# Optimization experiments

Measured on AMD Instinct MI355X. Metric: run time of the kernel, lower is better.

## Reference

```python
import jax, jax.numpy as jnp
import numpy as np

L, D, H, DH, DF = 4, 512, 8, 64, 2048
B, S = 4, 2048
EPS = 1e-6  # fast-transformers causal-linear eps


def _ln(x, g, b, eps=1e-5):
    mu = jnp.mean(x, axis=-1, keepdims=True)
    var = jnp.var(x, axis=-1, keepdims=True)
    return (x - mu) * jax.lax.rsqrt(var + eps) * g + b


def _causal_linear(Q, K, V):
    # Q, K, V: [B, S, H, DH]; O(N) linear-attention recurrence over S
    Qs = jnp.moveaxis(Q, 1, 0)
    Ks = jnp.moveaxis(K, 1, 0)
    Vs = jnp.moveaxis(V, 1, 0)
    b = Q.shape[0]
    kv0 = jnp.zeros((b, H, DH, DH), Q.dtype)  # running sum of k v^T
    z0 = jnp.zeros((b, H, DH), Q.dtype)       # running sum of k

    def step(carry, qkv):
        kv, z = carry
        q, k, v = qkv  # each [B, H, DH]
        kv = kv + k[..., :, None] * v[..., None, :]
        z = z + k
        num = jnp.einsum('bhd,bhdm->bhm', q, kv)
        den = jnp.einsum('bhd,bhd->bh', q, z) + EPS
        return (kv, z), num / den[..., None]

    _, out = jax.lax.scan(step, (kv0, z0), (Qs, Ks, Vs))
    return jnp.moveaxis(out, 0, 1)  # [B, S, H, DH]


def _layer(x, p):
    Wq, bq, Wk, bk, Wv, bv, Wo, bo, W1, b1, W2, b2, g1, be1, g2, be2 = p
    b, s, _ = x.shape
    q = (x @ Wq + bq).reshape(b, s, H, DH)
    k = (x @ Wk + bk).reshape(b, s, H, DH)
    v = (x @ Wv + bv).reshape(b, s, H, DH)
    Qf = jax.nn.elu(q) + 1.0  # feature map phi(x) = elu(x) + 1
    Kf = jax.nn.elu(k) + 1.0
    a = _causal_linear(Qf, Kf, v).reshape(b, s, D)
    x = x + (a @ Wo + bo)            # residual (dropout=0)
    x = _ln(x, g1, be1)              # post-norm
    y = jax.nn.gelu(x @ W1 + b1, approximate=False) @ W2 + b2
    return _ln(x + y, g2, be2)


def _encoder(h, params, gf, bef):
    def body(x, p):
        return _layer(x, p), None
    x, _ = jax.lax.scan(body, h, params)
    return _ln(x, gf, bef)  # final LayerNorm from builder


def setup_inputs() -> dict:
    key = jax.random.key(0)
    ks = jax.random.split(key, 8)

    def w(k, shape, fan_in):
        return jax.random.normal(k, shape, jnp.float32) * (fan_in ** -0.5)

    return {
        'h': jax.random.normal(ks[0], (B, S, D), jnp.float32),
        'Wq': w(ks[1], (L, D, D), D), 'bq': jnp.zeros((L, D), jnp.float32),
        'Wk': w(ks[2], (L, D, D), D), 'bk': jnp.zeros((L, D), jnp.float32),
        'Wv': w(ks[3], (L, D, D), D), 'bv': jnp.zeros((L, D), jnp.float32),
        'Wo': w(ks[4], (L, D, D), D), 'bo': jnp.zeros((L, D), jnp.float32),
        'W1': w(ks[5], (L, D, DF), D), 'b1': jnp.zeros((L, DF), jnp.float32),
        'W2': w(ks[6], (L, DF, D), DF), 'b2': jnp.zeros((L, D), jnp.float32),
        'g1': jnp.ones((L, D), jnp.float32), 'be1': jnp.zeros((L, D), jnp.float32),
        'g2': jnp.ones((L, D), jnp.float32), 'be2': jnp.zeros((L, D), jnp.float32),
        'gf': jnp.ones((D,), jnp.float32), 'bef': jnp.zeros((D,), jnp.float32),
    }


def reference(h, Wq, bq, Wk, bk, Wv, bv, Wo, bo, W1, b1, W2, b2,
              g1, be1, g2, be2, gf, bef):
    params = (Wq, bq, Wk, bk, Wv, bv, Wo, bo, W1, b1, W2, b2, g1, be1, g2, be2)
    return _encoder(h, params, gf, bef)
```

## Files before the change

kernel.cpp:

```cpp
#include <hip/hip_runtime.h>
#include <hip/hip_bf16.h>
#include <math.h>

#define LAYERS 4
#define DMODEL 512
#define NH 8
#define DH 64
#define DFF 2048
#define NB 4
#define S_LEN 2048
#define MROWS 8192
#define CHUNK 64
#define NCHUNK 32
#define ATT_EPS 1e-6f
#define LN_EPS 1e-5f
#define SEGSTRIDE (MROWS * DMODEL)

typedef __attribute__((ext_vector_type(8))) short short8v;
typedef __attribute__((ext_vector_type(4))) float f32x4;

__device__ __forceinline__ float b2f(unsigned short u) {
    union { float f; unsigned u; } c; c.u = ((unsigned)u) << 16; return c.f;
}
__device__ __forceinline__ unsigned short f2b(float f) {
    union { float f; unsigned u; } c; c.f = f;
    unsigned r = c.u + 0x7FFFu + ((c.u >> 16) & 1u);
    return (unsigned short)(r >> 16);
}
__device__ __forceinline__ void gload16(const void* g, void* l) {
    __builtin_amdgcn_global_load_lds(
        (const __attribute__((address_space(1))) void*)g,
        (__attribute__((address_space(3))) void*)l, 16, 0, 0);
}
__device__ __forceinline__ float elu1f(float v) {
    return (v > 0.f) ? (v + 1.f) : __expf(v);
}
__device__ __forceinline__ float geluf(float v) {
    float u = 0.7978845608028654f * v * (1.f + 0.044715f * v * v);
    float th = 1.f - 2.f / (1.f + __expf(2.f * u));
    return 0.5f * v * (1.f + th);
}

template <int ACT, bool ACCUM, bool ATOMIC, bool WF32, bool WBF16, int KSPLIT>
__global__ __launch_bounds__(512, 4) void gemm8(
    const unsigned short* __restrict__ A,
    const unsigned short* __restrict__ WT,
    const float* __restrict__ b0, const float* __restrict__ b1,
    const float* __restrict__ b2,
    float* __restrict__ C32, unsigned short* __restrict__ Cbf,
    int M, int N, int K)
{
    __shared__ short S[2][16384];

    const int t = threadIdx.x;
    const int m0 = blockIdx.x * 128, n0 = blockIdx.y * 128;
    const int kz = (KSPLIT > 1) ? blockIdx.z : 0;
    const int Kc = K / KSPLIT;
    const int kbeg = kz * Kc;
    const int lane = t & 63, wid = t >> 6;
    const int wm = (wid >> 2) * 64;
    const int wn = (wid & 3) * 32;
    const int fr = lane & 15, kg = lane >> 4;

    const unsigned short* gsrc[4];
    int ldso[4];
#pragma unroll
    for (int r = 0; r < 4; ++r) {
        const int u = (r & 1) ? (t + 512) : t;
        const bool isA = (r < 2);
        const int row = u >> 3, sp = u & 7, sl = sp ^ (row & 7);
        gsrc[r] = (isA ? A + (size_t)(m0 + row) * K
                       : WT + (size_t)(n0 + row) * K) + kbeg + sl * 8;
        ldso[r] = (isA ? 0 : 8192) + u * 8;
    }

    int aoff[2][4], boff[2][2];
#pragma unroll
    for (int h = 0; h < 2; ++h) {
#pragma unroll
        for (int m = 0; m < 4; ++m) {
            const int R = wm + m * 16 + fr;
            aoff[h][m] = R * 64 + (((h * 4 + kg) ^ (R & 7)) * 8);
        }
#pragma unroll
        for (int n = 0; n < 2; ++n) {
            const int R = wn + n * 16 + fr;
            boff[h][n] = 8192 + R * 64 + (((h * 4 + kg) ^ (R & 7)) * 8);
        }
    }

    f32x4 acc[4][2];
#pragma unroll
    for (int m = 0; m < 4; ++m)
#pragma unroll
        for (int n = 0; n < 2; ++n) acc[m][n] = (f32x4){0.f, 0.f, 0.f, 0.f};

#define STAGE(b, kt) do { _Pragma("unroll")                                  \
    for (int r = 0; r < 4; ++r)                                              \
        gload16(gsrc[r] + (size_t)(kt) * 64, &S[b][ldso[r]]); } while (0)

    const int NT = Kc >> 6;
    STAGE(0, 0);

    for (int td = 0; td < NT; ++td) {
        const int b = td & 1;
        if (td + 1 < NT) {
            STAGE(b ^ 1, td + 1);
            __builtin_amdgcn_sched_barrier(0);
            asm volatile("s_waitcnt vmcnt(4)");
        } else {
            __builtin_amdgcn_sched_barrier(0);
            asm volatile("s_waitcnt vmcnt(0)");
        }
        __builtin_amdgcn_sched_barrier(0);
        __builtin_amdgcn_s_barrier();
        __builtin_amdgcn_sched_barrier(0);

        short8v a0[4], b0f[2], a1[4], b1f[2];
#pragma unroll
        for (int m = 0; m < 4; ++m) a0[m] = *(const short8v*)&S[b][aoff[0][m]];
#pragma unroll
        for (int n = 0; n < 2; ++n) b0f[n] = *(const short8v*)&S[b][boff[0][n]];
#pragma unroll
        for (int m = 0; m < 4; ++m) a1[m] = *(const short8v*)&S[b][aoff[1][m]];
#pragma unroll
        for (int n = 0; n < 2; ++n) b1f[n] = *(const short8v*)&S[b][boff[1][n]];

        asm volatile("s_waitcnt lgkmcnt(6)");
        __builtin_amdgcn_sched_barrier(0);
        __builtin_amdgcn_s_setprio(1);
#pragma unroll
        for (int m = 0; m < 4; ++m)
#pragma unroll
            for (int n = 0; n < 2; ++n)
                acc[m][n] = __builtin_amdgcn_mfma_f32_16x16x32_bf16(
                    a0[m], b0f[n], acc[m][n], 0, 0, 0);
        __builtin_amdgcn_s_setprio(0);

        asm volatile("s_waitcnt lgkmcnt(0)");
        __builtin_amdgcn_sched_barrier(0);
        __builtin_amdgcn_s_setprio(1);
#pragma unroll
        for (int m = 0; m < 4; ++m)
#pragma unroll
            for (int n = 0; n < 2; ++n)
                acc[m][n] = __builtin_amdgcn_mfma_f32_16x16x32_bf16(
                    a1[m], b1f[n], acc[m][n], 0, 0, 0);
        __builtin_amdgcn_s_setprio(0);

        __builtin_amdgcn_sched_barrier(0);
        __builtin_amdgcn_s_barrier();
    }
#undef STAGE

    const int seg = (ACT == 3) ? (n0 >> 9) : 0;
    const float* bias = (ACT == 3) ? (seg == 0 ? b0 : (seg == 1 ? b1 : b2)) : b0;
    float bv[2];
#pragma unroll
    for (int n = 0; n < 2; ++n) {
        const int col = n0 + wn + n * 16 + fr;
        bv[n] = bias[(ACT == 3) ? (col - seg * 512) : col];
    }
    if (KSPLIT > 1 && kz != 0) { bv[0] = 0.f; bv[1] = 0.f; }

#pragma unroll
    for (int m = 0; m < 4; ++m)
#pragma unroll
        for (int n = 0; n < 2; ++n)
#pragma unroll
            for (int j = 0; j < 4; ++j) {
                const int row = m0 + wm + m * 16 + (lane >> 4) * 4 + j;
                const int col = n0 + wn + n * 16 + fr;
                float v = acc[m][n][j] + bv[n];
                if (ACCUM) v += C32[(size_t)row * N + col];
                if (ACT == 1) v = elu1f(v);
                else if (ACT == 2) v = geluf(v);
                else if (ACT == 3) { if (seg < 2) v = elu1f(v); }
                if (ATOMIC) {
                    atomicAdd(&C32[(size_t)row * N + col], v);
                } else {
                    if (WF32) C32[(size_t)row * N + col] = v;
                }
                if (WBF16) {
                    if (ACT == 3)
                        Cbf[(size_t)seg * SEGSTRIDE + (size_t)row * 512 + (col - seg * 512)] = f2b(v);
                    else
                        Cbf[(size_t)row * N + col] = f2b(v);
                }
            }
}

__global__ __launch_bounds__(256) void transpose_to_bf16(
    const float* __restrict__ W, unsigned short* __restrict__ WT, int K, int N)
{
    __shared__ float tile[32][33];
    const int k0 = blockIdx.x * 32, n0 = blockIdx.y * 32;
    const int tx = threadIdx.x & 31, ty = threadIdx.x >> 5;
#pragma unroll
    for (int i = ty; i < 32; i += 8)
        tile[i][tx] = W[(size_t)(k0 + i) * N + n0 + tx];
    __syncthreads();
#pragma unroll
    for (int i = ty; i < 32; i += 8)
        WT[(size_t)(n0 + i) * K + k0 + tx] = f2b(tile[tx][i]);
}

__global__ __launch_bounds__(256) void cvt_in(
    const float* __restrict__ h, float* __restrict__ x,
    unsigned short* __restrict__ xb, int n)
{
    const int i = (blockIdx.x * 256 + threadIdx.x) * 8;
    if (i >= n) return;
    f32x4 a = *(const f32x4*)(h + i);
    f32x4 b = *(const f32x4*)(h + i + 4);
    *(f32x4*)(x + i) = a;
    *(f32x4*)(x + i + 4) = b;
    short8v p;
    p[0] = f2b(a[0]); p[1] = f2b(a[1]); p[2] = f2b(a[2]); p[3] = f2b(a[3]);
    p[4] = f2b(b[0]); p[5] = f2b(b[1]); p[6] = f2b(b[2]); p[7] = f2b(b[3]);
    *(short8v*)(xb + i) = p;
}

__device__ __forceinline__ int swzo(int row, int sl) {
    return row * 64 + ((sl ^ (row & 7)) << 3);
}

__global__ __launch_bounds__(256) void attn_stage1(
    const unsigned short* __restrict__ Kf, const unsigned short* __restrict__ Vf,
    unsigned short* __restrict__ KVp, float* __restrict__ zp)
{
    const int c = blockIdx.x, hh = blockIdx.y, bb = blockIdx.z;
    const int t = threadIdx.x;
    const int lane = t & 63, w = t >> 6;
    const int fr = lane & 15, g = lane >> 4;

    __shared__ unsigned short KTs[64 * 72];
    __shared__ unsigned short VTs[64 * 72];

    const size_t rowbase = (size_t)(bb * S_LEN + c * CHUNK);
    const int colbase = hh * DH;

    {
        const int r = lane, cs = w * 16;
        const unsigned short* kp = Kf + (rowbase + r) * DMODEL + colbase + cs;
        const unsigned short* vp = Vf + (rowbase + r) * DMODEL + colbase + cs;
        short8v k0 = *(const short8v*)kp, k1 = *(const short8v*)(kp + 8);
        short8v v0 = *(const short8v*)vp, v1 = *(const short8v*)(vp + 8);
#pragma unroll
        for (int i = 0; i < 8; ++i) {
            KTs[(cs + i) * 72 + r]     = (unsigned short)k0[i];
            KTs[(cs + 8 + i) * 72 + r] = (unsigned short)k1[i];
            VTs[(cs + i) * 72 + r]     = (unsigned short)v0[i];
            VTs[(cs + 8 + i) * 72 + r] = (unsigned short)v1[i];
        }
    }
    __syncthreads();

    f32x4 cacc[4];
#pragma unroll
    for (int nf = 0; nf < 4; ++nf) cacc[nf] = (f32x4){0.f, 0.f, 0.f, 0.f};

    const short8v a0 = *(const short8v*)&VTs[(w * 16 + fr) * 72 + g * 8];
    const short8v a1 = *(const short8v*)&VTs[(w * 16 + fr) * 72 + (4 + g) * 8];
#pragma unroll
    for (int nf = 0; nf < 4; ++nf) {
        short8v bq0 = *(const short8v*)&KTs[(nf * 16 + fr) * 72 + g * 8];
        short8v bq1 = *(const short8v*)&KTs[(nf * 16 + fr) * 72 + (4 + g) * 8];
        cacc[nf] = __builtin_amdgcn_mfma_f32_16x16x32_bf16(a0, bq0, cacc[nf], 0, 0, 0);
        cacc[nf] = __builtin_amdgcn_mfma_f32_16x16x32_bf16(a1, bq1, cacc[nf], 0, 0, 0);
    }

    const size_t base = ((size_t)(bb * NH + hh) * NCHUNK + c) * (DH * DH);
#pragma unroll
    for (int nf = 0; nf < 4; ++nf)
#pragma unroll
        for (int reg = 0; reg < 4; ++reg) {
            const int e = w * 16 + g * 4 + reg;
            const int d = nf * 16 + fr;
            KVp[base + e * 64 + d] = f2b(cacc[nf][reg]);
        }

    if (t < 64) {
        float s = 0.f;
#pragma unroll
        for (int sl = 0; sl < 8; ++sl) {
            short8v kv = *(const short8v*)&KTs[t * 72 + sl * 8];
#pragma unroll
            for (int i = 0; i < 8; ++i) s += b2f((unsigned short)kv[i]);
        }
        zp[((size_t)(bb * NH + hh) * NCHUNK + c) * DH + t] = s;
    }
}

__global__ __launch_bounds__(256) void attn_stage2(
    const unsigned short* __restrict__ KVp, unsigned short* __restrict__ KVb,
    float* __restrict__ zp)
{
    const int bh = blockIdx.x;
    const int e = blockIdx.y * 256 + threadIdx.x;
    const size_t base = (size_t)bh * NCHUNK * (DH * DH) + e;
    float run = 0.f;
#pragma unroll 4
    for (int c = 0; c < NCHUNK; ++c) {
        const float tmp = b2f(KVp[base + (size_t)c * (DH * DH)]);
        KVb[base + (size_t)c * (DH * DH)] = f2b(run);
        run += tmp;
    }
    if (blockIdx.y == 0 && threadIdx.x < DH) {
        float rz = 0.f;
        const size_t zb = (size_t)bh * NCHUNK * DH + threadIdx.x;
#pragma unroll 4
        for (int c = 0; c < NCHUNK; ++c) {
            const float tmp = zp[zb + c * DH];
            zp[zb + c * DH] = rz;
            rz += tmp;
        }
    }
}

__global__ __launch_bounds__(256) void attn_stage3(
    const unsigned short* __restrict__ Qf, const unsigned short* __restrict__ Kf,
    const unsigned short* __restrict__ Vf, const unsigned short* __restrict__ KVb,
    const float* __restrict__ zp, unsigned short* __restrict__ Af)
{
    const int c = blockIdx.x, hh = blockIdx.y, bb = blockIdx.z;
    const int t = threadIdx.x;
    const int lane = t & 63, w = t >> 6;
    const int fr = lane & 15, g = lane >> 4;

    __shared__ unsigned short Qs[4096];
    __shared__ unsigned short Ks[4096];
    __shared__ unsigned short KVts[4096];
    __shared__ unsigned short VTs[64 * 72];
    __shared__ unsigned short Ps[64 * 72];
    __shared__ float zsh[DH];
    __shared__ float den_lds[64];

    const size_t rowbase = (size_t)(bb * S_LEN + c * CHUNK);
    const int colbase = hh * DH;
    const size_t kvbase = ((size_t)(bb * NH + hh) * NCHUNK + c) * (DH * DH);

#pragma unroll
    for (int iss = 0; iss < 2; ++iss) {
        const int u = iss * 256 + t, row = u >> 3, sl = u & 7;
        const int ssl = (sl ^ (row & 7)) * 8;
        gload16(Qf + (rowbase + row) * DMODEL + colbase + ssl, &Qs[(size_t)u * 8]);
        gload16(Kf + (rowbase + row) * DMODEL + colbase + ssl, &Ks[(size_t)u * 8]);
        gload16(KVb + kvbase + row * 64 + ssl, &KVts[(size_t)u * 8]);
    }
    {
        const int r = lane, cs = w * 16;
        const unsigned short* vp = Vf + (rowbase + r) * DMODEL + colbase + cs;
        short8v v0 = *(const short8v*)vp, v1 = *(const short8v*)(vp + 8);
#pragma unroll
        for (int i = 0; i < 8; ++i) {
            VTs[(cs + i) * 72 + r]     = (unsigned short)v0[i];
            VTs[(cs + 8 + i) * 72 + r] = (unsigned short)v1[i];
        }
    }
    if (t < DH) zsh[t] = zp[((size_t)(bb * NH + hh) * NCHUNK + c) * DH + t];
    __syncthreads();

    f32x4 c1[4];
#pragma unroll
    for (int mf = 0; mf < 4; ++mf) c1[mf] = (f32x4){0.f, 0.f, 0.f, 0.f};
    {
        const short8v bq0 = *(const short8v*)&Qs[swzo(w * 16 + fr, g)];
        const short8v bq1 = *(const short8v*)&Qs[swzo(w * 16 + fr, 4 + g)];
#pragma unroll
        for (int mf = 0; mf < 4; ++mf) {
            short8v ak0 = *(const short8v*)&Ks[swzo(mf * 16 + fr, g)];
            short8v ak1 = *(const short8v*)&Ks[swzo(mf * 16 + fr, 4 + g)];
            c1[mf] = __builtin_amdgcn_mfma_f32_16x16x32_bf16(ak0, bq0, c1[mf], 0, 0, 0);
            c1[mf] = __builtin_amdgcn_mfma_f32_16x16x32_bf16(ak1, bq1, c1[mf], 0, 0, 0);
        }
    }

    const int i_my = w * 16 + fr;
    float dint = 0.f;
#pragma unroll
    for (int mf = 0; mf < 4; ++mf)
#pragma unroll
        for (int reg = 0; reg < 4; ++reg) {
            const int j = mf * 16 + g * 4 + reg;
            const float v = (j <= i_my) ? c1[mf][reg] : 0.f;
            dint += v;
            Ps[i_my * 72 + j] = f2b(v);
        }
    dint += __shfl_xor(dint, 16);
    dint += __shfl_xor(dint, 32);

    float dpre = 0.f;
#pragma unroll
    for (int sl = 0; sl < 8; ++sl) {
        short8v qv = *(const short8v*)&Qs[swzo(i_my, sl)];
#pragma unroll
        for (int e = 0; e < 8; ++e) dpre += b2f((unsigned short)qv[e]) * zsh[sl * 8 + e];
    }
    if (g == 0) den_lds[i_my] = dpre + dint + ATT_EPS;

    f32x4 acc[4];
#pragma unroll
    for (int nf = 0; nf < 4; ++nf) acc[nf] = (f32x4){0.f, 0.f, 0.f, 0.f};
    {
        const short8v aq0 = *(const short8v*)&Qs[swzo(w * 16 + fr, g)];
        const short8v aq1 = *(const short8v*)&Qs[swzo(w * 16 + fr, 4 + g)];
#pragma unroll
        for (int nf = 0; nf < 4; ++nf) {
            short8v bkv0 = *(const short8v*)&KVts[swzo(nf * 16 + fr, g)];
            short8v bkv1 = *(const short8v*)&KVts[swzo(nf * 16 + fr, 4 + g)];
            acc[nf] = __builtin_amdgcn_mfma_f32_16x16x32_bf16(aq0, bkv0, acc[nf], 0, 0, 0);
            acc[nf] = __builtin_amdgcn_mfma_f32_16x16x32_bf16(aq1, bkv1, acc[nf], 0, 0, 0);
        }
        const short8v ap0 = *(const short8v*)&Ps[(w * 16 + fr) * 72 + g * 8];
        const short8v ap1 = *(const short8v*)&Ps[(w * 16 + fr) * 72 + (4 + g) * 8];
#pragma unroll
        for (int nf = 0; nf < 4; ++nf) {
            short8v bv0 = *(const short8v*)&VTs[(nf * 16 + fr) * 72 + g * 8];
            short8v bv1 = *(const short8v*)&VTs[(nf * 16 + fr) * 72 + (4 + g) * 8];
            acc[nf] = __builtin_amdgcn_mfma_f32_16x16x32_bf16(ap0, bv0, acc[nf], 0, 0, 0);
            acc[nf] = __builtin_amdgcn_mfma_f32_16x16x32_bf16(ap1, bv1, acc[nf], 0, 0, 0);
        }
    }

#pragma unroll
    for (int reg = 0; reg < 4; ++reg) {
        const int i = w * 16 + g * 4 + reg;
        const float inv = 1.f / den_lds[i];
        unsigned short* dst = Af + (rowbase + i) * DMODEL + colbase;
#pragma unroll
        for (int nf = 0; nf < 4; ++nf)
            dst[nf * 16 + fr] = f2b(acc[nf][reg] * inv);
    }
}

__global__ __launch_bounds__(256) void ln_kernel(float* __restrict__ X,
                                                 const float* __restrict__ g,
                                                 const float* __restrict__ b,
                                                 unsigned short* __restrict__ Xb)
{
    const size_t row = blockIdx.x * 4 + (threadIdx.x >> 6);
    const int t = threadIdx.x & 63;
    float* xr = X + row * DMODEL;
    f32x4 x0 = *(const f32x4*)&xr[t * 4];
    f32x4 x1 = *(const f32x4*)&xr[256 + t * 4];

    float s  = x0[0] + x0[1] + x0[2] + x0[3] + x1[0] + x1[1] + x1[2] + x1[3];
    float sq = x0[0]*x0[0] + x0[1]*x0[1] + x0[2]*x0[2] + x0[3]*x0[3] +
               x1[0]*x1[0] + x1[1]*x1[1] + x1[2]*x1[2] + x1[3]*x1[3];
#pragma unroll
    for (int m = 1; m < 64; m <<= 1) {
        s  += __shfl_xor(s, m);
        sq += __shfl_xor(sq, m);
    }
    const float mu  = s * (1.f / DMODEL);
    const float var = sq * (1.f / DMODEL) - mu * mu;
    const float rr  = rsqrtf(var + LN_EPS);

    const int c0 = t * 4, c1 = 256 + t * 4;
    f32x4 g0 = *(const f32x4*)&g[c0], g1v = *(const f32x4*)&g[c1];
    f32x4 b0 = *(const f32x4*)&b[c0], b1v = *(const f32x4*)&b[c1];
    f32x4 y0, y1;
#pragma unroll
    for (int i = 0; i < 4; ++i) {
        y0[i] = (x0[i] - mu) * rr * g0[i] + b0[i];
        y1[i] = (x1[i] - mu) * rr * g1v[i] + b1v[i];
    }
    *(f32x4*)&xr[c0] = y0;
    *(f32x4*)&xr[c1] = y1;
    if (Xb) {
        unsigned short* xb = Xb + row * DMODEL;
        ushort4 u0, u1;
        u0.x = f2b(y0[0]); u0.y = f2b(y0[1]); u0.z = f2b(y0[2]); u0.w = f2b(y0[3]);
        u1.x = f2b(y1[0]); u1.y = f2b(y1[1]); u1.z = f2b(y1[2]); u1.w = f2b(y1[3]);
        *(ushort4*)&xb[c0] = u0;
        *(ushort4*)&xb[c1] = u1;
    }
}

extern "C" void kernel_launch(void* const* d_in, const int* in_sizes, int n_in,
                              void* d_out, int out_size, void* d_ws, size_t ws_size,
                              hipStream_t stream)
{
    const float* h   = (const float*)d_in[0];
    const float* Wq  = (const float*)d_in[1];
    const float* bq  = (const float*)d_in[2];
    const float* Wk  = (const float*)d_in[3];
    const float* bk  = (const float*)d_in[4];
    const float* Wv  = (const float*)d_in[5];
    const float* bv  = (const float*)d_in[6];
    const float* Wo  = (const float*)d_in[7];
    const float* bo  = (const float*)d_in[8];
    const float* W1  = (const float*)d_in[9];
    const float* b1  = (const float*)d_in[10];
    const float* W2  = (const float*)d_in[11];
    const float* b2  = (const float*)d_in[12];
    const float* g1  = (const float*)d_in[13];
    const float* be1 = (const float*)d_in[14];
    const float* g2  = (const float*)d_in[15];
    const float* be2 = (const float*)d_in[16];
    const float* gf  = (const float*)d_in[17];
    const float* bef = (const float*)d_in[18];

    float* x = (float*)d_out;
    char* ws = (char*)d_ws;
    const size_t MB = 1024 * 1024;
    unsigned short* x_bf = (unsigned short*)(ws);
    unsigned short* qkv  = (unsigned short*)(ws + 8 * MB);
    unsigned short* qb   = qkv;
    unsigned short* kb   = qkv + SEGSTRIDE;
    unsigned short* vb   = qkv + 2 * (size_t)SEGSTRIDE;
    unsigned short* ab   = (unsigned short*)(ws + 32 * MB);
    unsigned short* hid  = (unsigned short*)(ws + 8 * MB);
    unsigned short* KVp  = (unsigned short*)(ws + 40 * MB);
    unsigned short* KVb  = (unsigned short*)(ws + 48 * MB);
    float* zp            = (float*)(ws + 56 * MB);
    unsigned short* WTall = (unsigned short*)(ws + 57 * MB);

    const int M = MROWS, D = DMODEL, DF = DFF;
    const size_t LSTR = 3 * 1024 * 1024;

    cvt_in<<<dim3(M * D / (256 * 8)), 256, 0, stream>>>(h, x, x_bf, M * D);
    for (int l = 0; l < LAYERS; ++l) {
        unsigned short* WL = WTall + (size_t)l * LSTR;
        transpose_to_bf16<<<dim3(D / 32, D / 32), 256, 0, stream>>>(Wq + (size_t)l * D * D, WL, D, D);
        transpose_to_bf16<<<dim3(D / 32, D / 32), 256, 0, stream>>>(Wk + (size_t)l * D * D, WL + 262144, D, D);
        transpose_to_bf16<<<dim3(D / 32, D / 32), 256, 0, stream>>>(Wv + (size_t)l * D * D, WL + 524288, D, D);
        transpose_to_bf16<<<dim3(D / 32, D / 32), 256, 0, stream>>>(Wo + (size_t)l * D * D, WL + 786432, D, D);
        transpose_to_bf16<<<dim3(D / 32, DF / 32), 256, 0, stream>>>(W1 + (size_t)l * D * DF, WL + 1048576, D, DF);
        transpose_to_bf16<<<dim3(DF / 32, D / 32), 256, 0, stream>>>(W2 + (size_t)l * DF * D, WL + 2097152, DF, D);
    }

    for (int l = 0; l < LAYERS; ++l) {
        unsigned short* WL = WTall + (size_t)l * LSTR;
        const unsigned short* WqkvT = WL;
        const unsigned short* WoT   = WL + 786432;
        const unsigned short* W1T   = WL + 1048576;
        const unsigned short* W2T   = WL + 2097152;

        gemm8<3, false, false, false, true, 1>
            <<<dim3(M / 128, 1536 / 128), 512, 0, stream>>>(
            x_bf, WqkvT, bq + (size_t)l * D, bk + (size_t)l * D, bv + (size_t)l * D,
            nullptr, qkv, M, 1536, D);

        attn_stage1<<<dim3(NCHUNK, NH, NB), 256, 0, stream>>>(kb, vb, KVp, zp);
        attn_stage2<<<dim3(NB * NH, 16), 256, 0, stream>>>(KVp, KVb, zp);
        attn_stage3<<<dim3(NCHUNK, NH, NB), 256, 0, stream>>>(qb, kb, vb, KVb, zp, ab);

        gemm8<0, true, false, true, false, 1>
            <<<dim3(M / 128, D / 128), 512, 0, stream>>>(
            ab, WoT, bo + (size_t)l * D, nullptr, nullptr, x, nullptr, M, D, D);
        ln_kernel<<<dim3(M / 4), 256, 0, stream>>>(x, g1 + (size_t)l * D, be1 + (size_t)l * D, x_bf);

        gemm8<2, false, false, false, true, 1>
            <<<dim3(M / 128, DF / 128), 512, 0, stream>>>(
            x_bf, W1T, b1 + (size_t)l * DF, nullptr, nullptr, nullptr, hid, M, DF, D);
        gemm8<0, false, true, false, false, 2>
            <<<dim3(M / 128, D / 128, 2), 512, 0, stream>>>(
            hid, W2T, b2 + (size_t)l * D, nullptr, nullptr, x, nullptr, M, D, DF);
        ln_kernel<<<dim3(M / 4), 256, 0, stream>>>(x, g2 + (size_t)l * D, be2 + (size_t)l * D, x_bf);
    }

    ln_kernel<<<dim3(M / 4), 256, 0, stream>>>(x, gf, bef, nullptr);
}
```

Baseline: 660.5 us.

## Switch GEMM to 256-thread blocks with 64x64 warp tiles and BK=32

The GEMM kernel moves from 8 waves per block (64x32 warp tiles, K-step 64) to 4 waves per block, each computing a 64x64 tile with a K-step of 32. This halves LDS use per block and raises register reuse of the fragments loaded from LDS. The LDS swizzle is adapted to the 32-wide rows. The out-projection GEMM also changes from a read-accumulate into x to a 2-way K-split that adds into x with atomics. In exchange there are more k-iterations with barriers, more registers per thread, and atomic traffic on the Wo output.

```diff
diff --git a/kernel.cpp b/kernel.cpp
--- a/kernel.cpp
+++ b/kernel.cpp
@@ -42,7 +42,7 @@
 }
 
 template <int ACT, bool ACCUM, bool ATOMIC, bool WF32, bool WBF16, int KSPLIT>
-__global__ __launch_bounds__(512, 4) void gemm8(
+__global__ __launch_bounds__(256, 4) void gemm4(
     const unsigned short* __restrict__ A,
     const unsigned short* __restrict__ WT,
     const float* __restrict__ b0, const float* __restrict__ b1,
@@ -50,7 +50,7 @@
     float* __restrict__ C32, unsigned short* __restrict__ Cbf,
     int M, int N, int K)
 {
-    __shared__ short S[2][16384];
+    __shared__ short S[2][8192];
 
     const int t = threadIdx.x;
     const int m0 = blockIdx.x * 128, n0 = blockIdx.y * 128;
@@ -58,48 +58,44 @@
     const int Kc = K / KSPLIT;
     const int kbeg = kz * Kc;
     const int lane = t & 63, wid = t >> 6;
-    const int wm = (wid >> 2) * 64;
-    const int wn = (wid & 3) * 32;
+    const int wm = (wid >> 1) * 64, wn = (wid & 1) * 64;
     const int fr = lane & 15, kg = lane >> 4;
 
     const unsigned short* gsrc[4];
     int ldso[4];
 #pragma unroll
     for (int r = 0; r < 4; ++r) {
-        const int u = (r & 1) ? (t + 512) : t;
+        const int u = (r & 1) ? (t + 256) : t;
         const bool isA = (r < 2);
-        const int row = u >> 3, sp = u & 7, sl = sp ^ (row & 7);
+        const int row = u >> 2, sp = u & 3, sl = sp ^ ((row >> 1) & 3);
         gsrc[r] = (isA ? A + (size_t)(m0 + row) * K
                        : WT + (size_t)(n0 + row) * K) + kbeg + sl * 8;
-        ldso[r] = (isA ? 0 : 8192) + u * 8;
-    }
-
-    int aoff[2][4], boff[2][2];
-#pragma unroll
-    for (int h = 0; h < 2; ++h) {
-#pragma unroll
-        for (int m = 0; m < 4; ++m) {
-            const int R = wm + m * 16 + fr;
-            aoff[h][m] = R * 64 + (((h * 4 + kg) ^ (R & 7)) * 8);
-        }
-#pragma unroll
-        for (int n = 0; n < 2; ++n) {
-            const int R = wn + n * 16 + fr;
-            boff[h][n] = 8192 + R * 64 + (((h * 4 + kg) ^ (R & 7)) * 8);
-        }
-    }
-
-    f32x4 acc[4][2];
+        ldso[r] = (isA ? 0 : 4096) + u * 8;
+    }
+
+    int aoff[4], boff[4];
+#pragma unroll
+    for (int m = 0; m < 4; ++m) {
+        const int R = wm + m * 16 + fr;
+        aoff[m] = R * 32 + ((kg ^ ((R >> 1) & 3)) << 3);
+    }
+#pragma unroll
+    for (int n = 0; n < 4; ++n) {
+        const int R = wn + n * 16 + fr;
+        boff[n] = 4096 + R * 32 + ((kg ^ ((R >> 1) & 3)) << 3);
+    }
+
+    f32x4 acc[4][4];
 #pragma unroll
     for (int m = 0; m < 4; ++m)
 #pragma unroll
-        for (int n = 0; n < 2; ++n) acc[m][n] = (f32x4){0.f, 0.f, 0.f, 0.f};
+        for (int n = 0; n < 4; ++n) acc[m][n] = (f32x4){0.f, 0.f, 0.f, 0.f};
 
 #define STAGE(b, kt) do { _Pragma("unroll")                                  \
     for (int r = 0; r < 4; ++r)                                              \
-        gload16(gsrc[r] + (size_t)(kt) * 64, &S[b][ldso[r]]); } while (0)
-
-    const int NT = Kc >> 6;
+        gload16(gsrc[r] + (size_t)(kt) * 32, &S[b][ldso[r]]); } while (0)
+
+    const int NT = Kc >> 5;
     STAGE(0, 0);
 
     for (int td = 0; td < NT; ++td) {
@@ -116,26 +112,11 @@
         __builtin_amdgcn_s_barrier();
         __builtin_amdgcn_sched_barrier(0);
 
-        short8v a0[4], b0f[2], a1[4], b1f[2];
-#pragma unroll
-        for (int m = 0; m < 4; ++m) a0[m] = *(const short8v*)&S[b][aoff[0][m]];
-#pragma unroll
-        for (int n = 0; n < 2; ++n) b0f[n] = *(const short8v*)&S[b][boff[0][n]];
-#pragma unroll
-        for (int m = 0; m < 4; ++m) a1[m] = *(const short8v*)&S[b][aoff[1][m]];
-#pragma unroll
-        for (int n = 0; n < 2; ++n) b1f[n] = *(const short8v*)&S[b][boff[1][n]];
-
-        asm volatile("s_waitcnt lgkmcnt(6)");
-        __builtin_amdgcn_sched_barrier(0);
-        __builtin_amdgcn_s_setprio(1);
-#pragma unroll
-        for (int m = 0; m < 4; ++m)
-#pragma unroll
-            for (int n = 0; n < 2; ++n)
-                acc[m][n] = __builtin_amdgcn_mfma_f32_16x16x32_bf16(
-                    a0[m], b0f[n], acc[m][n], 0, 0, 0);
-        __builtin_amdgcn_s_setprio(0);
+        short8v af[4], bf[4];
+#pragma unroll
+        for (int m = 0; m < 4; ++m) af[m] = *(const short8v*)&S[b][aoff[m]];
+#pragma unroll
+        for (int n = 0; n < 4; ++n) bf[n] = *(const short8v*)&S[b][boff[n]];
 
         asm volatile("s_waitcnt lgkmcnt(0)");
         __builtin_amdgcn_sched_barrier(0);
@@ -143,9 +124,9 @@
 #pragma unroll
         for (int m = 0; m < 4; ++m)
 #pragma unroll
-            for (int n = 0; n < 2; ++n)
+            for (int n = 0; n < 4; ++n)
                 acc[m][n] = __builtin_amdgcn_mfma_f32_16x16x32_bf16(
-                    a1[m], b1f[n], acc[m][n], 0, 0, 0);
+                    af[m], bf[n], acc[m][n], 0, 0, 0);
         __builtin_amdgcn_s_setprio(0);
 
         __builtin_amdgcn_sched_barrier(0);
@@ -155,18 +136,21 @@
 
     const int seg = (ACT == 3) ? (n0 >> 9) : 0;
     const float* bias = (ACT == 3) ? (seg == 0 ? b0 : (seg == 1 ? b1 : b2)) : b0;
-    float bv[2];
-#pragma unroll
-    for (int n = 0; n < 2; ++n) {
+    float bv[4];
+#pragma unroll
+    for (int n = 0; n < 4; ++n) {
         const int col = n0 + wn + n * 16 + fr;
         bv[n] = bias[(ACT == 3) ? (col - seg * 512) : col];
     }
-    if (KSPLIT > 1 && kz != 0) { bv[0] = 0.f; bv[1] = 0.f; }
+    if (KSPLIT > 1 && kz != 0) {
+#pragma unroll
+        for (int n = 0; n < 4; ++n) bv[n] = 0.f;
+    }
 
 #pragma unroll
     for (int m = 0; m < 4; ++m)
 #pragma unroll
-        for (int n = 0; n < 2; ++n)
+        for (int n = 0; n < 4; ++n)
 #pragma unroll
             for (int j = 0; j < 4; ++j) {
                 const int row = m0 + wm + m * 16 + (lane >> 4) * 4 + j;
@@ -538,8 +522,8 @@
         const unsigned short* W1T   = WL + 1048576;
         const unsigned short* W2T   = WL + 2097152;
 
-        gemm8<3, false, false, false, true, 1>
-            <<<dim3(M / 128, 1536 / 128), 512, 0, stream>>>(
+        gemm4<3, false, false, false, true, 1>
+            <<<dim3(M / 128, 1536 / 128), 256, 0, stream>>>(
             x_bf, WqkvT, bq + (size_t)l * D, bk + (size_t)l * D, bv + (size_t)l * D,
             nullptr, qkv, M, 1536, D);
 
@@ -547,16 +531,16 @@
         attn_stage2<<<dim3(NB * NH, 16), 256, 0, stream>>>(KVp, KVb, zp);
         attn_stage3<<<dim3(NCHUNK, NH, NB), 256, 0, stream>>>(qb, kb, vb, KVb, zp, ab);
 
-        gemm8<0, true, false, true, false, 1>
-            <<<dim3(M / 128, D / 128), 512, 0, stream>>>(
+        gemm4<0, false, true, false, false, 2>
+            <<<dim3(M / 128, D / 128, 2), 256, 0, stream>>>(
             ab, WoT, bo + (size_t)l * D, nullptr, nullptr, x, nullptr, M, D, D);
         ln_kernel<<<dim3(M / 4), 256, 0, stream>>>(x, g1 + (size_t)l * D, be1 + (size_t)l * D, x_bf);
 
-        gemm8<2, false, false, false, true, 1>
-            <<<dim3(M / 128, DF / 128), 512, 0, stream>>>(
+        gemm4<2, false, false, false, true, 1>
+            <<<dim3(M / 128, DF / 128), 256, 0, stream>>>(
             x_bf, W1T, b1 + (size_t)l * DF, nullptr, nullptr, nullptr, hid, M, DF, D);
-        gemm8<0, false, true, false, false, 2>
-            <<<dim3(M / 128, D / 128, 2), 512, 0, stream>>>(
+        gemm4<0, false, true, false, false, 2>
+            <<<dim3(M / 128, D / 128, 2), 256, 0, stream>>>(
             hid, W2T, b2 + (size_t)l * D, nullptr, nullptr, x, nullptr, M, D, DF);
         ln_kernel<<<dim3(M / 4), 256, 0, stream>>>(x, g2 + (size_t)l * D, be2 + (size_t)l * D, x_bf);
     }
```

Result: slower. 743.3 us (+12.5%).

## Carry residual stream in bf16 and fold residual add into GEMM epilogues

Applied to the files above, without the earlier changes.

Drops the fp32 copy of the hidden state. Each layer norm now writes only its bf16 output, and the Wo and W2 GEMM epilogues add the residual by reading that bf16 copy. An fp32 scratch buffer U, aliased over the attention KV workspace, receives the pre-norm sums. The first norm zeroes U so the split-K atomic W2 GEMM can accumulate into it. This is meant to cut fp32 read/write traffic on the residual path, at the cost of holding the residual in bf16 precision and adding an extra zeroing write.

```diff
diff --git a/kernel.cpp b/kernel.cpp
--- a/kernel.cpp
+++ b/kernel.cpp
@@ -41,13 +41,14 @@
     return 0.5f * v * (1.f + th);
 }
 
-template <int ACT, bool ACCUM, bool ATOMIC, bool WF32, bool WBF16, int KSPLIT>
+template <int ACT, bool RESID, bool ATOMIC, bool WU, bool WBF16, int KSPLIT>
 __global__ __launch_bounds__(512, 4) void gemm8(
     const unsigned short* __restrict__ A,
     const unsigned short* __restrict__ WT,
     const float* __restrict__ b0, const float* __restrict__ b1,
     const float* __restrict__ b2,
-    float* __restrict__ C32, unsigned short* __restrict__ Cbf,
+    const unsigned short* __restrict__ Xres,
+    float* __restrict__ U, unsigned short* __restrict__ Cbf,
     int M, int N, int K)
 {
     __shared__ short S[2][16384];
@@ -172,14 +173,15 @@
                 const int row = m0 + wm + m * 16 + (lane >> 4) * 4 + j;
                 const int col = n0 + wn + n * 16 + fr;
                 float v = acc[m][n][j] + bv[n];
-                if (ACCUM) v += C32[(size_t)row * N + col];
+                if (RESID && kz == 0)
+                    v += b2f(Xres[(size_t)row * 512 + col]);
                 if (ACT == 1) v = elu1f(v);
                 else if (ACT == 2) v = geluf(v);
                 else if (ACT == 3) { if (seg < 2) v = elu1f(v); }
                 if (ATOMIC) {
-                    atomicAdd(&C32[(size_t)row * N + col], v);
-                } else {
-                    if (WF32) C32[(size_t)row * N + col] = v;
+                    atomicAdd(&U[(size_t)row * N + col], v);
+                } else if (WU) {
+                    U[(size_t)row * N + col] = v;
                 }
                 if (WBF16) {
                     if (ACT == 3)
@@ -206,15 +208,12 @@
 }
 
 __global__ __launch_bounds__(256) void cvt_in(
-    const float* __restrict__ h, float* __restrict__ x,
-    unsigned short* __restrict__ xb, int n)
+    const float* __restrict__ h, unsigned short* __restrict__ xb, int n)
 {
     const int i = (blockIdx.x * 256 + threadIdx.x) * 8;
     if (i >= n) return;
     f32x4 a = *(const f32x4*)(h + i);
     f32x4 b = *(const f32x4*)(h + i + 4);
-    *(f32x4*)(x + i) = a;
-    *(f32x4*)(x + i + 4) = b;
     short8v p;
     p[0] = f2b(a[0]); p[1] = f2b(a[1]); p[2] = f2b(a[2]); p[3] = f2b(a[3]);
     p[4] = f2b(b[0]); p[5] = f2b(b[1]); p[6] = f2b(b[2]); p[7] = f2b(b[3]);
@@ -434,16 +433,17 @@
     }
 }
 
-__global__ __launch_bounds__(256) void ln_kernel(float* __restrict__ X,
-                                                 const float* __restrict__ g,
-                                                 const float* __restrict__ b,
-                                                 unsigned short* __restrict__ Xb)
+__global__ __launch_bounds__(256) void ln_u2x(float* __restrict__ U,
+                                              const float* __restrict__ g,
+                                              const float* __restrict__ b,
+                                              unsigned short* __restrict__ Xb,
+                                              int ZERO)
 {
     const size_t row = blockIdx.x * 4 + (threadIdx.x >> 6);
     const int t = threadIdx.x & 63;
-    float* xr = X + row * DMODEL;
-    f32x4 x0 = *(const f32x4*)&xr[t * 4];
-    f32x4 x1 = *(const f32x4*)&xr[256 + t * 4];
+    float* ur = U + row * DMODEL;
+    f32x4 x0 = *(const f32x4*)&ur[t * 4];
+    f32x4 x1 = *(const f32x4*)&ur[256 + t * 4];
 
     float s  = x0[0] + x0[1] + x0[2] + x0[3] + x1[0] + x1[1] + x1[2] + x1[3];
     float sq = x0[0]*x0[0] + x0[1]*x0[1] + x0[2]*x0[2] + x0[3]*x0[3] +
@@ -460,22 +460,58 @@
     const int c0 = t * 4, c1 = 256 + t * 4;
     f32x4 g0 = *(const f32x4*)&g[c0], g1v = *(const f32x4*)&g[c1];
     f32x4 b0 = *(const f32x4*)&b[c0], b1v = *(const f32x4*)&b[c1];
-    f32x4 y0, y1;
+    unsigned short* xb = Xb + row * DMODEL;
+    ushort4 u0, u1;
+    u0.x = f2b((x0[0] - mu) * rr * g0[0] + b0[0]);
+    u0.y = f2b((x0[1] - mu) * rr * g0[1] + b0[1]);
+    u0.z = f2b((x0[2] - mu) * rr * g0[2] + b0[2]);
+    u0.w = f2b((x0[3] - mu) * rr * g0[3] + b0[3]);
+    u1.x = f2b((x1[0] - mu) * rr * g1v[0] + b1v[0]);
+    u1.y = f2b((x1[1] - mu) * rr * g1v[1] + b1v[1]);
+    u1.z = f2b((x1[2] - mu) * rr * g1v[2] + b1v[2]);
+    u1.w = f2b((x1[3] - mu) * rr * g1v[3] + b1v[3]);
+    *(ushort4*)&xb[c0] = u0;
+    *(ushort4*)&xb[c1] = u1;
+    if (ZERO) {
+        *(f32x4*)&ur[c0] = (f32x4){0.f, 0.f, 0.f, 0.f};
+        *(f32x4*)&ur[c1] = (f32x4){0.f, 0.f, 0.f, 0.f};
+    }
+}
+
+__global__ __launch_bounds__(256) void ln_final(const unsigned short* __restrict__ Xb,
+                                                const float* __restrict__ g,
+                                                const float* __restrict__ b,
+                                                float* __restrict__ Out)
+{
+    const size_t row = blockIdx.x * 4 + (threadIdx.x >> 6);
+    const int t = threadIdx.x & 63;
+    const unsigned short* xr = Xb + row * DMODEL;
+    short8v xv = *(const short8v*)&xr[t * 8];
+    float x[8];
+#pragma unroll
+    for (int i = 0; i < 8; ++i) x[i] = b2f((unsigned short)xv[i]);
+
+    float s = 0.f, sq = 0.f;
+#pragma unroll
+    for (int i = 0; i < 8; ++i) { s += x[i]; sq += x[i] * x[i]; }
+#pragma unroll
+    for (int m = 1; m < 64; m <<= 1) {
+        s  += __shfl_xor(s, m);
+        sq += __shfl_xor(sq, m);
+    }
+    const float mu  = s * (1.f / DMODEL);
+    const float var = sq * (1.f / DMODEL) - mu * mu;
+    const float rr  = rsqrtf(var + LN_EPS);
+
+    float* orow = Out + row * DMODEL + t * 8;
+    f32x4 o0, o1;
 #pragma unroll
     for (int i = 0; i < 4; ++i) {
-        y0[i] = (x0[i] - mu) * rr * g0[i] + b0[i];
-        y1[i] = (x1[i] - mu) * rr * g1v[i] + b1v[i];
-    }
-    *(f32x4*)&xr[c0] = y0;
-    *(f32x4*)&xr[c1] = y1;
-    if (Xb) {
-        unsigned short* xb = Xb + row * DMODEL;
-        ushort4 u0, u1;
-        u0.x = f2b(y0[0]); u0.y = f2b(y0[1]); u0.z = f2b(y0[2]); u0.w = f2b(y0[3]);
-        u1.x = f2b(y1[0]); u1.y = f2b(y1[1]); u1.z = f2b(y1[2]); u1.w = f2b(y1[3]);
-        *(ushort4*)&xb[c0] = u0;
-        *(ushort4*)&xb[c1] = u1;
-    }
+        o0[i] = (x[i] - mu) * rr * g[t * 8 + i] + b[t * 8 + i];
+        o1[i] = (x[4 + i] - mu) * rr * g[t * 8 + 4 + i] + b[t * 8 + 4 + i];
+    }
+    *(f32x4*)orow = o0;
+    *(f32x4*)(orow + 4) = o1;
 }
 
 extern "C" void kernel_launch(void* const* d_in, const int* in_sizes, int n_in,
@@ -502,7 +538,6 @@
     const float* gf  = (const float*)d_in[17];
     const float* bef = (const float*)d_in[18];
 
-    float* x = (float*)d_out;
     char* ws = (char*)d_ws;
     const size_t MB = 1024 * 1024;
     unsigned short* x_bf = (unsigned short*)(ws);
@@ -514,13 +549,14 @@
     unsigned short* hid  = (unsigned short*)(ws + 8 * MB);
     unsigned short* KVp  = (unsigned short*)(ws + 40 * MB);
     unsigned short* KVb  = (unsigned short*)(ws + 48 * MB);
+    float* U             = (float*)(ws + 40 * MB);
     float* zp            = (float*)(ws + 56 * MB);
     unsigned short* WTall = (unsigned short*)(ws + 57 * MB);
 
     const int M = MROWS, D = DMODEL, DF = DFF;
     const size_t LSTR = 3 * 1024 * 1024;
 
-    cvt_in<<<dim3(M * D / (256 * 8)), 256, 0, stream>>>(h, x, x_bf, M * D);
+    cvt_in<<<dim3(M * D / (256 * 8)), 256, 0, stream>>>(h, x_bf, M * D);
     for (int l = 0; l < LAYERS; ++l) {
         unsigned short* WL = WTall + (size_t)l * LSTR;
         transpose_to_bf16<<<dim3(D / 32, D / 32), 256, 0, stream>>>(Wq + (size_t)l * D * D, WL, D, D);
@@ -541,7 +577,7 @@
         gemm8<3, false, false, false, true, 1>
             <<<dim3(M / 128, 1536 / 128), 512, 0, stream>>>(
             x_bf, WqkvT, bq + (size_t)l * D, bk + (size_t)l * D, bv + (size_t)l * D,
-            nullptr, qkv, M, 1536, D);
+            nullptr, nullptr, qkv, M, 1536, D);
 
         attn_stage1<<<dim3(NCHUNK, NH, NB), 256, 0, stream>>>(kb, vb, KVp, zp);
         attn_stage2<<<dim3(NB * NH, 16), 256, 0, stream>>>(KVp, KVb, zp);
@@ -549,17 +585,17 @@
 
         gemm8<0, true, false, true, false, 1>
             <<<dim3(M / 128, D / 128), 512, 0, stream>>>(
-            ab, WoT, bo + (size_t)l * D, nullptr, nullptr, x, nullptr, M, D, D);
-        ln_kernel<<<dim3(M / 4), 256, 0, stream>>>(x, g1 + (size_t)l * D, be1 + (size_t)l * D, x_bf);
+            ab, WoT, bo + (size_t)l * D, nullptr, nullptr, x_bf, U, nullptr, M, D, D);
+        ln_u2x<<<dim3(M / 4), 256, 0, stream>>>(U, g1 + (size_t)l * D, be1 + (size_t)l * D, x_bf, 1);
 
         gemm8<2, false, false, false, true, 1>
             <<<dim3(M / 128, DF / 128), 512, 0, stream>>>(
-            x_bf, W1T, b1 + (size_t)l * DF, nullptr, nullptr, nullptr, hid, M, DF, D);
-        gemm8<0, false, true, false, false, 2>
+            x_bf, W1T, b1 + (size_t)l * DF, nullptr, nullptr, nullptr, nullptr, hid, M, DF, D);
+        gemm8<0, true, true, false, false, 2>
             <<<dim3(M / 128, D / 128, 2), 512, 0, stream>>>(
-            hid, W2T, b2 + (size_t)l * D, nullptr, nullptr, x, nullptr, M, D, DF);
-        ln_kernel<<<dim3(M / 4), 256, 0, stream>>>(x, g2 + (size_t)l * D, be2 + (size_t)l * D, x_bf);
-    }
-
-    ln_kernel<<<dim3(M / 4), 256, 0, stream>>>(x, gf, bef, nullptr);
-}
+            hid, W2T, b2 + (size_t)l * D, nullptr, nullptr, x_bf, U, nullptr, M, D, DF);
+        ln_u2x<<<dim3(M / 4), 256, 0, stream>>>(U, g2 + (size_t)l * D, be2 + (size_t)l * D, x_bf, 0);
+    }
+
+    ln_final<<<dim3(M / 4), 256, 0, stream>>>(x_bf, gf, bef, (float*)d_out);
+}
```

Measured after the change: 637.3 us. 3.5% less time.
